# Optimization experiments

Hardware: AMD Instinct MI355X
Metric: run time of the kernel (lower is better)

The kernel has to match this reference:

```python
import jax, jax.numpy as jnp
import numpy as np

B, N, DIM = 4, 4096, 1024
HEADS, DIM_HEAD = 16, 64
DIM_INNER = HEADS * DIM_HEAD
ATTN_SCALE = 8.0
EPS = 1e-12  # F.normalize default eps


def setup_inputs() -> dict:
    key = jax.random.key(0)
    k1, k2, k3, k4, k5 = jax.random.split(key, 5)
    x = jax.random.normal(k1, (B, N, DIM), dtype=jnp.float32)
    gamma = jnp.ones((DIM,), dtype=jnp.float32)
    # stored as (in, out) so forward is x @ w
    w_qkv = jax.random.normal(k2, (DIM, 3 * DIM_INNER), dtype=jnp.float32) * (DIM ** -0.5)
    temperature = jnp.ones((HEADS, 1, 1), dtype=jnp.float32)
    w_out = jax.random.normal(k3, (DIM_INNER, DIM), dtype=jnp.float32) * (DIM_INNER ** -0.5)
    return {"x": x, "gamma": gamma, "w_qkv": w_qkv, "temperature": temperature, "w_out": w_out}


def _l2norm(t):
    # F.normalize(t, dim=-1): t / max(||t||_2, eps)
    n = jnp.linalg.norm(t, axis=-1, keepdims=True)
    return t / jnp.maximum(n, EPS)


def reference(x, gamma, w_qkv, temperature, w_out):
    b, n, dim = x.shape
    # RMSNorm: F.normalize(x, dim=-1) * sqrt(dim) * gamma
    xn = _l2norm(x) * (dim ** 0.5) * gamma
    # QKV projection -> qkv b h d n
    qkv = (xn @ w_qkv).reshape(b, n, 3, HEADS, DIM_HEAD)
    qkv = qkv.transpose(2, 0, 3, 4, 1)  # (3, b, h, d, n)
    q, k, v = qkv[0], qkv[1], qkv[2]
    # l2-normalize q, k over the sequence (last) axis; temperature-scale q
    q = _l2norm(q) * jnp.exp(temperature)  # temperature: (h,1,1) broadcast
    k = _l2norm(k)
    # cross-covariance attention over the small channel dim d
    sim = jnp.einsum('bhdn,bhen->bhde', q, k) * ATTN_SCALE
    attn = jax.nn.softmax(sim, axis=-1)
    out = jnp.einsum('bhde,bhen->bhdn', attn, v)
    # b h d n -> b n (h d), then out projection
    out = out.transpose(0, 3, 1, 2).reshape(b, n, DIM_INNER)
    return out @ w_out
```

## Files before the change

### kernel.cpp

```cpp
#include <hip/hip_runtime.h>
#include <stdint.h>

typedef unsigned short u16;
typedef unsigned int u32;
typedef __attribute__((ext_vector_type(8))) __bf16 bf16x8;
typedef __attribute__((ext_vector_type(4))) float f32x4;

#define M_TOT 16384
#define DIMX  1024

__device__ __forceinline__ u16 f2b(float f) {
  u32 u = __builtin_bit_cast(u32, f);
  u32 r = (u + 0x7fffu + ((u >> 16) & 1u)) >> 16;
  return (u16)r;
}

__device__ __forceinline__ void gl2lds16(const void* g, void* l) {
  __builtin_amdgcn_global_load_lds((const __attribute__((address_space(1))) void*)g,
                                   (__attribute__((address_space(3))) void*)l,
                                   16, 0, 0);
}

__global__ __launch_bounds__(256) void k_rms(const float* __restrict__ x,
                                             const float* __restrict__ gamma,
                                             u16* __restrict__ xn) {
  int row = blockIdx.x;
  int t = threadIdx.x;
  const float4* xr = (const float4*)(x + (size_t)row * DIMX);
  float4 v = xr[t];
  float ss = v.x * v.x + v.y * v.y + v.z * v.z + v.w * v.w;
#pragma unroll
  for (int o = 32; o > 0; o >>= 1) ss += __shfl_xor(ss, o, 64);
  __shared__ float wss[4];
  int w = t >> 6;
  if ((t & 63) == 0) wss[w] = ss;
  __syncthreads();
  float tot = wss[0] + wss[1] + wss[2] + wss[3];
  float scale = 32.0f / fmaxf(sqrtf(tot), 1e-12f);
  float4 g = ((const float4*)gamma)[t];
  ushort4 o4;
  o4.x = f2b(v.x * scale * g.x);
  o4.y = f2b(v.y * scale * g.y);
  o4.z = f2b(v.z * scale * g.z);
  o4.w = f2b(v.w * scale * g.w);
  ((ushort4*)xn)[(size_t)row * 256 + t] = o4;
}

__global__ __launch_bounds__(256) void k_castT(const float* __restrict__ in,
                                               u16* __restrict__ out, int Rr, int Cc) {
  __shared__ float tile[32][33];
  int c0 = blockIdx.x * 32, r0 = blockIdx.y * 32;
  int tx = threadIdx.x, ty = threadIdx.y;
#pragma unroll
  for (int i = 0; i < 4; i++)
    tile[ty + i * 8][tx] = in[(size_t)(r0 + ty + i * 8) * Cc + c0 + tx];
  __syncthreads();
#pragma unroll
  for (int i = 0; i < 4; i++)
    out[(size_t)(c0 + ty + i * 8) * Rr + r0 + tx] = f2b(tile[tx][ty + i * 8]);
}


template<bool SWAP>
__device__ __forceinline__ f32x4 mf(bf16x8 a, bf16x8 b, f32x4 c) {
  return SWAP ? __builtin_amdgcn_mfma_f32_16x16x32_bf16(b, a, c, 0, 0, 0)
              : __builtin_amdgcn_mfma_f32_16x16x32_bf16(a, b, c, 0, 0, 0);
}

__device__ __forceinline__ void stage128(const u16* __restrict__ g,
                                         u16* dst, int t, int k0) {
#pragma unroll
  for (int r = 0; r < 4; r++) {
    int c = r * 256 + t;
    int row = c >> 3;
    int sl = (c & 7) ^ (row & 7);
    gl2lds16(g + (size_t)row * 1024 + k0 + sl * 8,
             dst + (r * 256 + (t >> 6) * 64) * 8);
  }
}

template<bool SWAP>
__device__ __forceinline__ void gemm_core128(const u16* __restrict__ Ag,
                                             const u16* __restrict__ Bg,
                                             u16* lds, int t, f32x4 (&acc)[4][4]) {
  const int lane = t & 63;
  const int r16 = lane & 15, q = lane >> 4;
  const int s0 = (q ^ (r16 & 7)) * 8;
  const int wr = (t >> 6) >> 1, wc = (t >> 6) & 1;
  const int arow = wr * 64 + r16;
  const int brow = wc * 64 + r16;

  stage128(Ag, lds + 0,    t, 0);
  stage128(Bg, lds + 8192, t, 0);
  asm volatile("s_waitcnt vmcnt(0)" ::: "memory");
  __builtin_amdgcn_s_barrier();

  bf16x8 af[4][2], bf[4][2];
#pragma unroll 1
  for (int tt = 0; tt < 16; tt++) {
    const int bo = (tt & 1) << 14;
    const int nb = bo ^ 16384;
    const int k1 = ((tt + 1) & 15) << 6;
    stage128(Ag, lds + nb,        t, k1);
    stage128(Bg, lds + nb + 8192, t, k1);
    const u16* A = lds + bo;
    const u16* B = lds + bo + 8192;
#pragma unroll
    for (int i = 0; i < 4; i++) {
      af[i][0] = *(const bf16x8*)(A + (i * 16 + arow) * 64 + s0);
      af[i][1] = *(const bf16x8*)(A + (i * 16 + arow) * 64 + (s0 ^ 32));
      bf[i][0] = *(const bf16x8*)(B + (i * 16 + brow) * 64 + s0);
      bf[i][1] = *(const bf16x8*)(B + (i * 16 + brow) * 64 + (s0 ^ 32));
    }
    __builtin_amdgcn_s_setprio(1);
#pragma unroll
    for (int kq = 0; kq < 2; kq++)
#pragma unroll
      for (int i = 0; i < 4; i++)
#pragma unroll
        for (int j = 0; j < 4; j++)
          acc[i][j] = mf<SWAP>(af[i][kq], bf[j][kq], acc[i][j]);
    __builtin_amdgcn_s_setprio(0);
    asm volatile("s_waitcnt vmcnt(0)" ::: "memory");
    __builtin_amdgcn_s_barrier();
  }
}

__global__ __launch_bounds__(256, 2) void k_gemm1(const u16* __restrict__ A,
                                                  const u16* __restrict__ Bt,
                                                  u16* __restrict__ qkT,
                                                  u16* __restrict__ vmat,
                                                  float* __restrict__ sumsq) {
  __shared__ u16 lds[2 * 16384];
  int l = blockIdx.x;
  int xcd = l & 7, c = l >> 3;
  int mt = xcd * 16 + (c & 15);
  int nt = c >> 4;
  int m0 = mt * 128, n0 = nt * 128;
  int t = threadIdx.x, lane = t & 63;
  int r16 = lane & 15, q = lane >> 4;
  int wr = (t >> 6) >> 1, wc = (t >> 6) & 1;
  f32x4 acc[4][4] = {};
  if (n0 < 2048) {
    gemm_core128<false>(A + (size_t)m0 * 1024, Bt + (size_t)n0 * 1024, lds, t, acc);
    int b = m0 >> 12;
#pragma unroll
    for (int j = 0; j < 4; j++) {
      int cc = n0 + wc * 64 + j * 16 + r16;
      float colss = 0.f;
#pragma unroll
      for (int i = 0; i < 4; i++) {
        f32x4 a = acc[i][j];
        colss += a.x * a.x + a.y * a.y + a.z * a.z + a.w * a.w;
        int m = m0 + wr * 64 + i * 16 + q * 4;
        ushort4 o4;
        o4.x = f2b(a.x); o4.y = f2b(a.y); o4.z = f2b(a.z); o4.w = f2b(a.w);
        *(ushort4*)(qkT + (size_t)cc * M_TOT + m) = o4;
      }
      colss += __shfl_xor(colss, 16, 64);
      colss += __shfl_xor(colss, 32, 64);
      if (lane < 16) atomicAdd(&sumsq[b * 2048 + cc], colss);
    }
  } else {
    gemm_core128<true>(A + (size_t)m0 * 1024, Bt + (size_t)n0 * 1024, lds, t, acc);
    int vc0 = n0 - 2048;
#pragma unroll
    for (int i = 0; i < 4; i++) {
      int m = m0 + wr * 64 + i * 16 + r16;
#pragma unroll
      for (int j = 0; j < 4; j++) {
        int cc = vc0 + wc * 64 + j * 16 + q * 4;
        f32x4 a = acc[i][j];
        ushort4 o4;
        o4.x = f2b(a.x); o4.y = f2b(a.y); o4.z = f2b(a.z); o4.w = f2b(a.w);
        *(ushort4*)(vmat + (size_t)m * 1024 + cc) = o4;
      }
    }
  }
}

__global__ __launch_bounds__(256) void k_attn_s(const u16* __restrict__ qkT,
                                                float* __restrict__ Spart) {
  __shared__ u16 Ql[64 * 256];
  __shared__ u16 Kl[64 * 256];
  int bh = blockIdx.x, split = blockIdx.y;
  int b = bh >> 4, h = bh & 15;
  int t = threadIdx.x, lane = t & 63, w = t >> 6;
  int r16 = lane & 15, q = lane >> 4;
  const u16* qbase = qkT + (size_t)(h * 64) * M_TOT + b * 4096 + split * 1024;
  const u16* kbase = qkT + (size_t)(1024 + h * 64) * M_TOT + b * 4096 + split * 1024;
  int drow = w * 16 + r16;
  f32x4 acc[4] = {};
#pragma unroll 1
  for (int it = 0; it < 4; it++) {
    int ncol = it * 256;
#pragma unroll
    for (int r = 0; r < 8; r++) {
      int ch = r * 256 + t;
      int row = ch >> 5;
      int sl = (ch & 31) ^ (row & 31);
      gl2lds16(qbase + (size_t)row * M_TOT + ncol + sl * 8,
               Ql + (r * 256 + w * 64) * 8);
      gl2lds16(kbase + (size_t)row * M_TOT + ncol + sl * 8,
               Kl + (r * 256 + w * 64) * 8);
    }
    asm volatile("s_waitcnt vmcnt(0)" ::: "memory");
    __syncthreads();
#pragma unroll
    for (int it2 = 0; it2 < 8; it2++) {
      bf16x8 aq = *(const bf16x8*)(Ql + drow * 256 + (((it2 * 4 + q) ^ (drow & 31)) * 8));
#pragma unroll
      for (int j = 0; j < 4; j++) {
        int erow = j * 16 + r16;
        bf16x8 bk = *(const bf16x8*)(Kl + erow * 256 + (((it2 * 4 + q) ^ (erow & 31)) * 8));
        acc[j] = __builtin_amdgcn_mfma_f32_16x16x32_bf16(bk, aq, acc[j], 0, 0, 0);
      }
    }
    __syncthreads();
  }
  float* Sp = Spart + ((size_t)split * 64 + bh) * 4096;
#pragma unroll
  for (int j = 0; j < 4; j++)
    *(f32x4*)(Sp + drow * 64 + j * 16 + q * 4) = acc[j];
}

__global__ __launch_bounds__(256) void k_softmax(const float* __restrict__ Spart,
                                                 const float* __restrict__ sumsq,
                                                 const float* __restrict__ temp,
                                                 u16* __restrict__ PT) {
  int bh = blockIdx.x;
  int b = bh >> 4, h = bh & 15;
  int t = threadIdx.x;
  int d = t & 63, w = t >> 6;
  int e0 = w * 16;
  __shared__ float rnk[64];
  __shared__ float redm[4][64];
  __shared__ float reds[4][64];
  if (t < 64) rnk[t] = 1.0f / fmaxf(sqrtf(sumsq[b * 2048 + 1024 + h * 64 + t]), 1e-12f);
  __syncthreads();
  float nq = sqrtf(sumsq[b * 2048 + h * 64 + d]);
  float qs = 8.0f * __expf(temp[h]) / fmaxf(nq, 1e-12f);
  const float* Sp = Spart + (size_t)bh * 4096 + d * 64 + e0;
  float vals[16];
#pragma unroll
  for (int e = 0; e < 16; e += 4) {
    f32x4 v = {};
#pragma unroll
    for (int s = 0; s < 4; s++)
      v += *(const f32x4*)(Sp + (size_t)s * 64 * 4096 + e);
    vals[e + 0] = v.x; vals[e + 1] = v.y; vals[e + 2] = v.z; vals[e + 3] = v.w;
  }
  float mx = -3.0e38f;
#pragma unroll
  for (int e = 0; e < 16; e++) {
    float v = vals[e] * qs * rnk[e0 + e];
    vals[e] = v;
    mx = fmaxf(mx, v);
  }
  redm[w][d] = mx;
  __syncthreads();
  float M = fmaxf(fmaxf(redm[0][d], redm[1][d]), fmaxf(redm[2][d], redm[3][d]));
  float s = 0.f;
#pragma unroll
  for (int e = 0; e < 16; e++) {
    float v = __expf(vals[e] - M);
    vals[e] = v;
    s += v;
  }
  reds[w][d] = s;
  __syncthreads();
  float inv = 1.0f / (reds[0][d] + reds[1][d] + reds[2][d] + reds[3][d]);
#pragma unroll
  for (int e = 0; e < 16; e++)
    PT[((size_t)bh * 64 + e0 + e) * 64 + d] = f2b(vals[e] * inv);
}

__global__ __launch_bounds__(256) void k_m(const u16* __restrict__ woT,
                                           const u16* __restrict__ PT,
                                           u16* __restrict__ MT) {
  int bh = blockIdx.x;
  int b = bh >> 4, h = bh & 15;
  int o0 = blockIdx.y * 128;
  int t = threadIdx.x, lane = t & 63, w = t >> 6;
  int r16 = lane & 15, q = lane >> 4;
  const u16* pbase = PT + (size_t)bh * 4096;
  f32x4 acc[2][4] = {};
#pragma unroll
  for (int ks = 0; ks < 2; ks++) {
    int kk = ks * 32 + q * 8;
    bf16x8 af[2], bfr[4];
#pragma unroll
    for (int i = 0; i < 2; i++)
      af[i] = *(const bf16x8*)(woT + (size_t)(o0 + w * 32 + i * 16 + r16) * 1024 + h * 64 + kk);
#pragma unroll
    for (int j = 0; j < 4; j++)
      bfr[j] = *(const bf16x8*)(pbase + (size_t)(j * 16 + r16) * 64 + kk);
#pragma unroll
    for (int i = 0; i < 2; i++)
#pragma unroll
      for (int j = 0; j < 4; j++)
        acc[i][j] = __builtin_amdgcn_mfma_f32_16x16x32_bf16(af[i], bfr[j], acc[i][j], 0, 0, 0);
  }
  u16* dst = MT + (size_t)b * 1024 * 1024;
#pragma unroll
  for (int i = 0; i < 2; i++) {
    int o = o0 + w * 32 + i * 16 + q * 4;
#pragma unroll
    for (int j = 0; j < 4; j++) {
      int e = h * 64 + j * 16 + r16;
      f32x4 a = acc[i][j];
      dst[(size_t)(o + 0) * 1024 + e] = f2b(a.x);
      dst[(size_t)(o + 1) * 1024 + e] = f2b(a.y);
      dst[(size_t)(o + 2) * 1024 + e] = f2b(a.z);
      dst[(size_t)(o + 3) * 1024 + e] = f2b(a.w);
    }
  }
}

__global__ __launch_bounds__(256, 2) void k_gemm2(const u16* __restrict__ A,
                                                  const u16* __restrict__ Bt,
                                                  float* __restrict__ C) {
  __shared__ u16 lds[2 * 16384];
  int l = blockIdx.x;
  int xcd = l & 7, c = l >> 3;
  int mt = xcd * 16 + (c & 15);
  int nt = c >> 4;
  int m0 = mt * 128, n0 = nt * 128;
  int b = m0 >> 12;
  const u16* Bb = Bt + (size_t)b * 1024 * 1024;
  int t = threadIdx.x, lane = t & 63;
  int r16 = lane & 15, q = lane >> 4;
  int wr = (t >> 6) >> 1, wc = (t >> 6) & 1;
  f32x4 acc[4][4] = {};
  gemm_core128<true>(A + (size_t)m0 * 1024, Bb + (size_t)n0 * 1024, lds, t, acc);
#pragma unroll
  for (int i = 0; i < 4; i++) {
    int m = m0 + wr * 64 + i * 16 + r16;
#pragma unroll
    for (int j = 0; j < 4; j++) {
      int cc = n0 + wc * 64 + j * 16 + q * 4;
      *(f32x4*)(C + (size_t)m * 1024 + cc) = acc[i][j];
    }
  }
}

extern "C" void kernel_launch(void* const* d_in, const int* in_sizes, int n_in,
                              void* d_out, int out_size, void* d_ws, size_t ws_size,
                              hipStream_t stream) {
  const float* x     = (const float*)d_in[0];
  const float* gamma = (const float*)d_in[1];
  const float* wqkv  = (const float*)d_in[2];
  const float* temp  = (const float*)d_in[3];
  const float* wout  = (const float*)d_in[4];
  float* out = (float*)d_out;

  char* ws = (char*)d_ws;
  size_t off = 0;
  u16* xn = (u16*)(ws + off);    off += (size_t)M_TOT * 1024 * 2;
  u16* wqT = (u16*)(ws + off);   off += (size_t)3072 * 1024 * 2;
  u16* woT = (u16*)(ws + off);   off += (size_t)1024 * 1024 * 2;
  u16* qkT = (u16*)(ws + off);   off += (size_t)2048 * M_TOT * 2;
  u16* vmat = (u16*)(ws + off);  off += (size_t)M_TOT * 1024 * 2;
  float* sumsq = (float*)(ws + off); off += (size_t)4 * 2048 * 4;
  u16* PT = (u16*)(ws + off);    off += (size_t)64 * 64 * 64 * 2;
  u16* MT = (u16*)(ws + off);    off += (size_t)4 * 1024 * 1024 * 2;

  float* Spart = (float*)xn;

  hipMemsetAsync((void*)sumsq, 0, (size_t)4 * 2048 * 4, stream);

  k_rms<<<16384, 256, 0, stream>>>(x, gamma, xn);
  dim3 cb(32, 8);
  k_castT<<<dim3(3072 / 32, 1024 / 32), cb, 0, stream>>>(wqkv, wqT, 1024, 3072);
  k_castT<<<dim3(1024 / 32, 1024 / 32), cb, 0, stream>>>(wout, woT, 1024, 1024);
  k_gemm1<<<3072, 256, 0, stream>>>(xn, wqT, qkT, vmat, sumsq);
  k_attn_s<<<dim3(64, 4), 256, 0, stream>>>(qkT, Spart);
  k_softmax<<<64, 256, 0, stream>>>(Spart, sumsq, temp, PT);
  k_m<<<dim3(64, 8), 256, 0, stream>>>(woT, PT, MT);
  k_gemm2<<<1024, 256, 0, stream>>>(vmat, MT, out);
}
```

Before: 311.1 us.

## Use 256x128 GEMM tiles with 8 waves and K-step 32; merge weight casts

Both bf16 GEMMs move from 128x128 tiles with 4 waves and K-step 64 to 256x128 tiles with 8 waves (512 threads) and K-step 32, with launch bounds requesting 4 blocks per CU. Larger M tiles halve the number of blocks and share B-tile loads across more rows, aiming to cut global traffic and per-block overhead. The XOR swizzle in LDS is dropped for 64-byte rows, which risks LDS bank conflicts. The tight launch bound squeezes the register budget against a 64-float accumulator, which risks spilling. The two weight transpose-cast launches are also merged into one kernel.

```diff
diff --git a/kernel.cpp b/kernel.cpp
--- a/kernel.cpp
+++ b/kernel.cpp
@@ -46,10 +46,15 @@
   ((ushort4*)xn)[(size_t)row * 256 + t] = o4;
 }
 
-__global__ __launch_bounds__(256) void k_castT(const float* __restrict__ in,
-                                               u16* __restrict__ out, int Rr, int Cc) {
+__global__ __launch_bounds__(256) void k_castT2(const float* __restrict__ wqkv,
+                                                const float* __restrict__ wout,
+                                                u16* __restrict__ wqT,
+                                                u16* __restrict__ woT) {
   __shared__ float tile[32][33];
-  int c0 = blockIdx.x * 32, r0 = blockIdx.y * 32;
+  const float* in; u16* out; int Cc; int c0;
+  if (blockIdx.x < 96) { in = wqkv; out = wqT; Cc = 3072; c0 = blockIdx.x * 32; }
+  else                 { in = wout; out = woT; Cc = 1024; c0 = (blockIdx.x - 96) * 32; }
+  int r0 = blockIdx.y * 32;
   int tx = threadIdx.x, ty = threadIdx.y;
 #pragma unroll
   for (int i = 0; i < 4; i++)
@@ -57,7 +62,7 @@
   __syncthreads();
 #pragma unroll
   for (int i = 0; i < 4; i++)
-    out[(size_t)(c0 + ty + i * 8) * Rr + r0 + tx] = f2b(tile[tx][ty + i * 8]);
+    out[(size_t)(c0 + ty + i * 8) * 1024 + r0 + tx] = f2b(tile[tx][ty + i * 8]);
 }
 
 
@@ -67,82 +72,82 @@
               : __builtin_amdgcn_mfma_f32_16x16x32_bf16(a, b, c, 0, 0, 0);
 }
 
-__device__ __forceinline__ void stage128(const u16* __restrict__ g,
-                                         u16* dst, int t, int k0) {
-#pragma unroll
-  for (int r = 0; r < 4; r++) {
-    int c = r * 256 + t;
-    int row = c >> 3;
-    int sl = (c & 7) ^ (row & 7);
-    gl2lds16(g + (size_t)row * 1024 + k0 + sl * 8,
-             dst + (r * 256 + (t >> 6) * 64) * 8);
+__device__ __forceinline__ void stage_ab(const u16* __restrict__ Ag,
+                                         const u16* __restrict__ Bg,
+                                         u16* dstA, u16* dstB, int t, int k0) {
+#pragma unroll
+  for (int r = 0; r < 2; r++) {
+    int c = r * 512 + t;
+    int row = c >> 2, slot = c & 3;
+    gl2lds16(Ag + (size_t)row * 1024 + k0 + slot * 8,
+             dstA + (r * 512 + (t >> 6) * 64) * 8);
+  }
+  {
+    int row = t >> 2, slot = t & 3;
+    gl2lds16(Bg + (size_t)row * 1024 + k0 + slot * 8,
+             dstB + ((t >> 6) * 64) * 8);
   }
 }
 
 template<bool SWAP>
-__device__ __forceinline__ void gemm_core128(const u16* __restrict__ Ag,
-                                             const u16* __restrict__ Bg,
-                                             u16* lds, int t, f32x4 (&acc)[4][4]) {
+__device__ __forceinline__ void gemm_core(const u16* __restrict__ Ag,
+                                          const u16* __restrict__ Bg,
+                                          u16* lds, int t, f32x4 (&acc)[4][4]) {
   const int lane = t & 63;
   const int r16 = lane & 15, q = lane >> 4;
-  const int s0 = (q ^ (r16 & 7)) * 8;
   const int wr = (t >> 6) >> 1, wc = (t >> 6) & 1;
   const int arow = wr * 64 + r16;
   const int brow = wc * 64 + r16;
-
-  stage128(Ag, lds + 0,    t, 0);
-  stage128(Bg, lds + 8192, t, 0);
+  u16* A0 = lds;               u16* B0 = lds + 8192;
+  u16* A1 = lds + 12288;       u16* B1 = lds + 12288 + 8192;
+
+  stage_ab(Ag, Bg, A0, B0, t, 0);
   asm volatile("s_waitcnt vmcnt(0)" ::: "memory");
   __builtin_amdgcn_s_barrier();
 
-  bf16x8 af[4][2], bf[4][2];
+  bf16x8 af[4], bf[4];
 #pragma unroll 1
-  for (int tt = 0; tt < 16; tt++) {
-    const int bo = (tt & 1) << 14;
-    const int nb = bo ^ 16384;
-    const int k1 = ((tt + 1) & 15) << 6;
-    stage128(Ag, lds + nb,        t, k1);
-    stage128(Bg, lds + nb + 8192, t, k1);
-    const u16* A = lds + bo;
-    const u16* B = lds + bo + 8192;
+  for (int tt = 0; tt < 32; tt++) {
+    const int cur = (tt & 1) ? 12288 : 0;
+    const int nxt = cur ^ 12288;
+    const int k1 = ((tt + 1) & 31) << 5;
+    stage_ab(Ag, Bg, lds + nxt, lds + nxt + 8192, t, k1);
+    const u16* A = lds + cur;
+    const u16* B = lds + cur + 8192;
 #pragma unroll
     for (int i = 0; i < 4; i++) {
-      af[i][0] = *(const bf16x8*)(A + (i * 16 + arow) * 64 + s0);
-      af[i][1] = *(const bf16x8*)(A + (i * 16 + arow) * 64 + (s0 ^ 32));
-      bf[i][0] = *(const bf16x8*)(B + (i * 16 + brow) * 64 + s0);
-      bf[i][1] = *(const bf16x8*)(B + (i * 16 + brow) * 64 + (s0 ^ 32));
+      af[i] = *(const bf16x8*)(A + (i * 16 + arow) * 32 + q * 8);
+      bf[i] = *(const bf16x8*)(B + (i * 16 + brow) * 32 + q * 8);
     }
     __builtin_amdgcn_s_setprio(1);
 #pragma unroll
-    for (int kq = 0; kq < 2; kq++)
-#pragma unroll
-      for (int i = 0; i < 4; i++)
-#pragma unroll
-        for (int j = 0; j < 4; j++)
-          acc[i][j] = mf<SWAP>(af[i][kq], bf[j][kq], acc[i][j]);
+    for (int i = 0; i < 4; i++)
+#pragma unroll
+      for (int j = 0; j < 4; j++)
+        acc[i][j] = mf<SWAP>(af[i], bf[j], acc[i][j]);
     __builtin_amdgcn_s_setprio(0);
     asm volatile("s_waitcnt vmcnt(0)" ::: "memory");
     __builtin_amdgcn_s_barrier();
   }
 }
 
-__global__ __launch_bounds__(256, 2) void k_gemm1(const u16* __restrict__ A,
+__global__ __launch_bounds__(512, 4) void k_gemm1(const u16* __restrict__ A,
                                                   const u16* __restrict__ Bt,
                                                   u16* __restrict__ qkT,
                                                   u16* __restrict__ vmat,
                                                   float* __restrict__ sumsq) {
-  __shared__ u16 lds[2 * 16384];
+  __shared__ u16 lds[2 * 12288];
   int l = blockIdx.x;
   int xcd = l & 7, c = l >> 3;
-  int mt = xcd * 16 + (c & 15);
-  int nt = c >> 4;
-  int m0 = mt * 128, n0 = nt * 128;
+  int mt = xcd * 8 + (c & 7);
+  int nt = c >> 3;
+  int m0 = mt * 256, n0 = nt * 128;
   int t = threadIdx.x, lane = t & 63;
   int r16 = lane & 15, q = lane >> 4;
   int wr = (t >> 6) >> 1, wc = (t >> 6) & 1;
   f32x4 acc[4][4] = {};
   if (n0 < 2048) {
-    gemm_core128<false>(A + (size_t)m0 * 1024, Bt + (size_t)n0 * 1024, lds, t, acc);
+    gemm_core<false>(A + (size_t)m0 * 1024, Bt + (size_t)n0 * 1024, lds, t, acc);
     int b = m0 >> 12;
 #pragma unroll
     for (int j = 0; j < 4; j++) {
@@ -162,7 +167,7 @@
       if (lane < 16) atomicAdd(&sumsq[b * 2048 + cc], colss);
     }
   } else {
-    gemm_core128<true>(A + (size_t)m0 * 1024, Bt + (size_t)n0 * 1024, lds, t, acc);
+    gemm_core<true>(A + (size_t)m0 * 1024, Bt + (size_t)n0 * 1024, lds, t, acc);
     int vc0 = n0 - 2048;
 #pragma unroll
     for (int i = 0; i < 4; i++) {
@@ -317,22 +322,22 @@
   }
 }
 
-__global__ __launch_bounds__(256, 2) void k_gemm2(const u16* __restrict__ A,
+__global__ __launch_bounds__(512, 4) void k_gemm2(const u16* __restrict__ A,
                                                   const u16* __restrict__ Bt,
                                                   float* __restrict__ C) {
-  __shared__ u16 lds[2 * 16384];
+  __shared__ u16 lds[2 * 12288];
   int l = blockIdx.x;
   int xcd = l & 7, c = l >> 3;
-  int mt = xcd * 16 + (c & 15);
-  int nt = c >> 4;
-  int m0 = mt * 128, n0 = nt * 128;
+  int mt = xcd * 8 + (c & 7);
+  int nt = c >> 3;
+  int m0 = mt * 256, n0 = nt * 128;
   int b = m0 >> 12;
   const u16* Bb = Bt + (size_t)b * 1024 * 1024;
   int t = threadIdx.x, lane = t & 63;
   int r16 = lane & 15, q = lane >> 4;
   int wr = (t >> 6) >> 1, wc = (t >> 6) & 1;
   f32x4 acc[4][4] = {};
-  gemm_core128<true>(A + (size_t)m0 * 1024, Bb + (size_t)n0 * 1024, lds, t, acc);
+  gemm_core<true>(A + (size_t)m0 * 1024, Bb + (size_t)n0 * 1024, lds, t, acc);
 #pragma unroll
   for (int i = 0; i < 4; i++) {
     int m = m0 + wr * 64 + i * 16 + r16;
@@ -371,11 +376,10 @@
 
   k_rms<<<16384, 256, 0, stream>>>(x, gamma, xn);
   dim3 cb(32, 8);
-  k_castT<<<dim3(3072 / 32, 1024 / 32), cb, 0, stream>>>(wqkv, wqT, 1024, 3072);
-  k_castT<<<dim3(1024 / 32, 1024 / 32), cb, 0, stream>>>(wout, woT, 1024, 1024);
-  k_gemm1<<<3072, 256, 0, stream>>>(xn, wqT, qkT, vmat, sumsq);
+  k_castT2<<<dim3(128, 32), cb, 0, stream>>>(wqkv, wout, wqT, woT);
+  k_gemm1<<<1536, 512, 0, stream>>>(xn, wqT, qkT, vmat, sumsq);
   k_attn_s<<<dim3(64, 4), 256, 0, stream>>>(qkT, Spart);
   k_softmax<<<64, 256, 0, stream>>>(Spart, sumsq, temp, PT);
   k_m<<<dim3(64, 8), 256, 0, stream>>>(woT, PT, MT);
-  k_gemm2<<<1024, 256, 0, stream>>>(vmat, MT, out);
-}
+  k_gemm2<<<512, 512, 0, stream>>>(vmat, MT, out);
+}
```

Result: slower. 324.4 us (+4.3%).
